# Performance work log

Hardware: AMD Instinct MI355X
Metric: run time of the kernel (lower is better)

Reference implementation:

```python
import jax, jax.numpy as jnp
import numpy as np

B, T, D, H = 64, 1024, 1, 256  # batch, seq_len, input_size(=output_size), hidden_size


def setup_inputs() -> dict:
    key = jax.random.key(0)
    ks = jax.random.split(key, 16)
    s = 1.0 / np.sqrt(H)  # torch LSTM/Linear default uniform init scale
    u = lambda k, shp: jax.random.uniform(k, shp, jnp.float32, -s, s)
    return {
        "x": jax.random.normal(ks[0], (B, T, D), jnp.float32),
        # encoder bidirectional 2-layer LSTM; leading dim 2 = (fwd, bwd); gate order i,f,g,o
        "enc_Wih_l0": u(ks[1], (2, 4 * H, D)),
        "enc_Whh_l0": u(ks[2], (2, 4 * H, H)),
        "enc_b_l0": u(ks[3], (2, 4 * H)),
        "enc_Wih_l1": u(ks[4], (2, 4 * H, 2 * H)),
        "enc_Whh_l1": u(ks[5], (2, 4 * H, H)),
        "enc_b_l1": u(ks[6], (2, 4 * H)),
        # decoder bidirectional 2-layer LSTM
        "dec_Wih_l0": u(ks[7], (2, 4 * H, D)),
        "dec_Whh_l0": u(ks[8], (2, 4 * H, H)),
        "dec_b_l0": u(ks[9], (2, 4 * H)),
        "dec_Wih_l1": u(ks[10], (2, 4 * H, 2 * H)),
        "dec_Whh_l1": u(ks[11], (2, 4 * H, H)),
        "dec_b_l1": u(ks[12], (2, 4 * H)),
        # output projection: Linear(2H -> 1)
        "fc_W": u(ks[13], (1, 2 * H)),
        "fc_b": u(ks[14], (1,)),
    }


def _cell(xt, h, c, Wih, Whh, b):
    # one LSTM cell step; xt: (B, Din), h/c: (B, H)
    gates = xt @ Wih.T + h @ Whh.T + b
    i, f, g, o = jnp.split(gates, 4, axis=-1)  # torch gate order i,f,g,o
    c = jax.nn.sigmoid(f) * c + jax.nn.sigmoid(i) * jnp.tanh(g)
    h = jax.nn.sigmoid(o) * jnp.tanh(c)
    return h, c


def _scan_dir(xs, Wih, Whh, b, reverse):
    # xs: (T, B, Din) time-major; returns (T,B,H) outputs aligned to input order + final (h,c)
    bsz = xs.shape[1]
    h0 = jnp.zeros((bsz, H), xs.dtype)
    def step(carry, xt):
        h, c = _cell(xt, carry[0], carry[1], Wih, Whh, b)
        return (h, c), h
    (hT, cT), ys = jax.lax.scan(step, (h0, h0), xs, reverse=reverse)
    return ys, hT, cT


def reference(x, enc_Wih_l0, enc_Whh_l0, enc_b_l0, enc_Wih_l1, enc_Whh_l1, enc_b_l1,
              dec_Wih_l0, dec_Whh_l0, dec_b_l0, dec_Wih_l1, dec_Whh_l1, dec_b_l1,
              fc_W, fc_b):
    xT = jnp.transpose(x, (1, 0, 2))  # (T, B, D)
    # ---- encoder: 2-layer bidirectional LSTM, zero initial state ----
    yf0, hf0, cf0 = _scan_dir(xT, enc_Wih_l0[0], enc_Whh_l0[0], enc_b_l0[0], False)
    yb0, hb0, cb0 = _scan_dir(xT, enc_Wih_l0[1], enc_Whh_l0[1], enc_b_l0[1], True)
    y0 = jnp.concatenate([yf0, yb0], axis=-1)  # (T, B, 2H)
    _, hf1, cf1 = _scan_dir(y0, enc_Wih_l1[0], enc_Whh_l1[0], enc_b_l1[0], False)
    _, hb1, cb1 = _scan_dir(y0, enc_Wih_l1[1], enc_Whh_l1[1], enc_b_l1[1], True)
    # torch state layout: [l0_fwd, l0_bwd, l1_fwd, l1_bwd]
    eh = (hf0, hb0, hf1, hb1)
    ec = (cf0, cb0, cf1, cb1)

    # ---- decoder: each step re-initializes LSTM state from ENCODER state (source bug,
    # reproduced faithfully); only the fc output feeds back as the next input ----
    def dec_step(x_in, _):
        hf, _c1 = _cell(x_in, eh[0], ec[0], dec_Wih_l0[0], dec_Whh_l0[0], dec_b_l0[0])
        hb, _c2 = _cell(x_in, eh[1], ec[1], dec_Wih_l0[1], dec_Whh_l0[1], dec_b_l0[1])
        z = jnp.concatenate([hf, hb], axis=-1)  # (B, 2H)
        hf1_, _c3 = _cell(z, eh[2], ec[2], dec_Wih_l1[0], dec_Whh_l1[0], dec_b_l1[0])
        hb1_, _c4 = _cell(z, eh[3], ec[3], dec_Wih_l1[1], dec_Whh_l1[1], dec_b_l1[1])
        y = jnp.concatenate([hf1_, hb1_], axis=-1) @ fc_W.T + fc_b  # (B, 1)
        return y, y

    x0 = jnp.zeros((x.shape[0], x.shape[2]), x.dtype)
    _, ys = jax.lax.scan(dec_step, x0, None, length=x.shape[1])  # (T, B, 1)
    return jnp.transpose(ys, (1, 0, 2))  # (B, T, 1)
```

## Files before the change

kernel.cpp:

```cpp
#include <hip/hip_runtime.h>
#include <hip/hip_bf16.h>
#include <hip/hip_fp16.h>
#include <math.h>


#define NWG 256
#define THR 512
#define U0S 132

#define ECL0   2048
#define EHL1   (ECL0 + 32768)
#define ECL1   (EHL1 + 16384)
#define ROF    (ECL1 + 32768)
#define WIH1T  (ROF + 262144)
#define GWR    (WIH1T + 524288)
#define PCF    (GWR + 1048576)
#define Y0OF   (PCF + 8192)
#define WS_REQ_BYTES ((size_t)(Y0OF + 16777216) * 4)

struct SeqParams {
  const void *x, *eWih0, *eWhh0, *eB0, *eWih1, *eWhh1, *eB1;
  const void *dWih0, *dWhh0, *dB0, *dWih1, *dWhh1, *dB1, *fcW, *fcb;
  void* out;
  float* ws;
  unsigned* ctrs;
};

typedef _Float16 hlf2 __attribute__((ext_vector_type(2)));

__device__ __forceinline__ float bf2f(unsigned short u) {
  return __uint_as_float(((unsigned)u) << 16);
}
__device__ __forceinline__ float hf2f(unsigned short u) {
  __half_raw r; r.x = u; return __half2float(__half(r));
}
__device__ __forceinline__ unsigned short f2h_u(float f) {
  __half h = __float2half(f);
  return *reinterpret_cast<unsigned short*>(&h);
}

__device__ __forceinline__ float fexp2(float x) {
#if __has_builtin(__builtin_amdgcn_exp2f)
  return __builtin_amdgcn_exp2f(x);
#else
  return exp2f(x);
#endif
}
__device__ __forceinline__ float frcp(float x) {
#if __has_builtin(__builtin_amdgcn_rcpf)
  return __builtin_amdgcn_rcpf(x);
#else
  return 1.0f / x;
#endif
}
__device__ __forceinline__ float sigm(float v) {
  return frcp(1.0f + fexp2(v * -1.44269504f));
}
__device__ __forceinline__ float ftanh(float v) {
  return fmaf(-2.0f, frcp(1.0f + fexp2(v * 2.88539008f)), 1.0f);
}

#if __has_builtin(__builtin_amdgcn_fdot2)
__device__ __forceinline__ float fdot2(hlf2 a, hlf2 b, float c) {
  return __builtin_amdgcn_fdot2(a, b, c, false);
}
#else
__device__ __forceinline__ float fdot2(hlf2 a, hlf2 b, float c) {
  return c + (float)a[0] * (float)b[0] + (float)a[1] * (float)b[1];
}
#endif

__device__ __forceinline__ float dot1(float a, const uint4& x, const uint4& y) {
  const hlf2* xp = reinterpret_cast<const hlf2*>(&x);
  const hlf2* yp = reinterpret_cast<const hlf2*>(&y);
  a = fdot2(xp[0], yp[0], a);
  a = fdot2(xp[1], yp[1], a);
  a = fdot2(xp[2], yp[2], a);
  a = fdot2(xp[3], yp[3], a);
  return a;
}
__device__ __forceinline__ void dot2acc(float4& a, const uint4& hv, const uint4& wv) {
  const hlf2* hp = reinterpret_cast<const hlf2*>(&hv);
  const hlf2* wp = reinterpret_cast<const hlf2*>(&wv);
  a.x = fdot2(hp[0], wp[0], a.x);
  a.y = fdot2(hp[1], wp[1], a.y);
  a.z = fdot2(hp[2], wp[2], a.z);
  a.w = fdot2(hp[3], wp[3], a.w);
}

__device__ __forceinline__ float ldin(const void* p_, size_t i, int bf) {
  return bf ? bf2f(((const unsigned short*)p_)[i]) : ((const float*)p_)[i];
}
__device__ __forceinline__ void stout(void* o, size_t i, float v, int bf) {
  if (bf) ((__hip_bfloat16*)o)[i] = __float2bfloat16(v);
  else    ((float*)o)[i] = v;
}

__device__ __forceinline__ int detect_bf16(const void* xp) {
  const unsigned* u = (const unsigned*)xp;
  int votes = 0;
#pragma unroll 8
  for (int i = 0; i < 64; ++i) {
    unsigned e = (u[i] >> 7) & 0xFF;
    votes += (e >= 108 && e <= 131) ? 1 : 0;
  }
  return votes >= 32;
}

__device__ __forceinline__ void gbar(unsigned* ctrs, unsigned gen) {
  __syncthreads();
  if (threadIdx.x == 0) {
    __hip_atomic_fetch_add(&ctrs[(blockIdx.x & 31) * 32], 1u,
                           __ATOMIC_RELEASE, __HIP_MEMORY_SCOPE_AGENT);
  }
  if (threadIdx.x < 32) {
    while (__hip_atomic_load(&ctrs[threadIdx.x * 32], __ATOMIC_RELAXED,
                             __HIP_MEMORY_SCOPE_AGENT) < gen * 8u) {
      __builtin_amdgcn_s_sleep(1);
    }
    (void)__hip_atomic_load(&ctrs[threadIdx.x * 32], __ATOMIC_ACQUIRE,
                            __HIP_MEMORY_SCOPE_AGENT);
  }
  __syncthreads();
}

__device__ __forceinline__ uint4 ldw8(const void* src, size_t off, int bf) {
  union { __half h[8]; uint4 u; } r;
  if (bf) {
    const unsigned short* s = (const unsigned short*)src + off;
    ushort4 a = *reinterpret_cast<const ushort4*>(s);
    ushort4 b = *reinterpret_cast<const ushort4*>(s + 4);
    r.h[0] = __float2half(bf2f(a.x)); r.h[1] = __float2half(bf2f(a.y));
    r.h[2] = __float2half(bf2f(a.z)); r.h[3] = __float2half(bf2f(a.w));
    r.h[4] = __float2half(bf2f(b.x)); r.h[5] = __float2half(bf2f(b.y));
    r.h[6] = __float2half(bf2f(b.z)); r.h[7] = __float2half(bf2f(b.w));
  } else {
    const float* s = (const float*)src + off;
    float4 a = *reinterpret_cast<const float4*>(s);
    float4 b = *reinterpret_cast<const float4*>(s + 4);
    r.h[0] = __float2half(a.x); r.h[1] = __float2half(a.y);
    r.h[2] = __float2half(a.z); r.h[3] = __float2half(a.w);
    r.h[4] = __float2half(b.x); r.h[5] = __float2half(b.y);
    r.h[6] = __float2half(b.z); r.h[7] = __float2half(b.w);
  }
  return r.u;
}

__device__ __forceinline__ void stage_u128(unsigned* AH, const unsigned* src,
                                           int ustr, int uoff) {
  const int t = threadIdx.x;
#pragma unroll
  for (int i = 0; i < 4; ++i) {
    int idx = t + i * THR;
    int r = idx >> 5, c4 = (idx & 31) << 2;
    uint4 v = *reinterpret_cast<const uint4*>(src + (size_t)r * ustr + uoff + c4);
    *reinterpret_cast<uint4*>(AH + r * U0S + c4) = v;
  }
}
__device__ __forceinline__ void load_w16_rows(uint4 (&wr)[2][4], const void* src,
                                              int rowbase, int bf) {
  const int t = threadIdx.x, kc = t >> 6, rt = t & 3;
#pragma unroll
  for (int j = 0; j < 2; ++j) {
    size_t rb = (size_t)(rowbase + rt * 2 + j) * 256 + kc * 32;
#pragma unroll
    for (int d = 0; d < 4; ++d) wr[j][d] = ldw8(src, rb + d * 8, bf);
  }
}
__device__ __forceinline__ void dot2_t4(float4* acc, const unsigned* A,
                                        const uint4 (&wr)[2][4]) {
  const int t = threadIdx.x;
  const int kc = t >> 6, bt = (t & 63) >> 2;
#pragma unroll
  for (int d = 0; d < 4; ++d) {
    const int k = kc * 16 + d * 4;
    uint4 h0 = *reinterpret_cast<const uint4*>(A + (bt +  0) * U0S + k);
    uint4 h1 = *reinterpret_cast<const uint4*>(A + (bt + 16) * U0S + k);
    uint4 h2 = *reinterpret_cast<const uint4*>(A + (bt + 32) * U0S + k);
    uint4 h3 = *reinterpret_cast<const uint4*>(A + (bt + 48) * U0S + k);
    dot2acc(acc[0], h0, wr[0][d]); dot2acc(acc[1], h0, wr[1][d]);
    dot2acc(acc[2], h1, wr[0][d]); dot2acc(acc[3], h1, wr[1][d]);
    dot2acc(acc[4], h2, wr[0][d]); dot2acc(acc[5], h2, wr[1][d]);
    dot2acc(acc[6], h3, wr[0][d]); dot2acc(acc[7], h3, wr[1][d]);
  }
}
__device__ __forceinline__ void reduce_R(const float4* acc, float* part, float* dst,
                                         const void* bsrc, int rowbase, int bf) {
  const int t = threadIdx.x;
  const int kc = t >> 6, tile = t & 63;
#pragma unroll
  for (int e = 0; e < 8; ++e) {
    const float4 a = acc[e];
    part[e * 512 + kc * 64 + tile] = (a.x + a.y) + (a.z + a.w);
  }
  __syncthreads();
  {
    const int r = t >> 6, b = t & 63;
    const int tl = (b & 15) * 4 + (r >> 1);
    const float* pp = part + ((b >> 4) * 2 + (r & 1)) * 512 + tl;
    float v = ((pp[0] + pp[64]) + (pp[128] + pp[192])) +
              ((pp[256] + pp[320]) + (pp[384] + pp[448]));
    dst[(size_t)b * 1024 + rowbase + r] = v + ldin(bsrc, rowbase + r, bf);
  }
  __syncthreads();
}

__global__ void __launch_bounds__(THR, 2)
__attribute__((amdgpu_waves_per_eu(2, 2)))
seq2seq_kernel(SeqParams p) {
  __shared__ __align__(16) char smem[148736];
  uint4* WLDSu4 = (uint4*)smem;
  float* GF     = (float*)(smem + 131072);
  float* PREB   = (float*)(smem + 135168);
  float* PREWf  = (float*)(smem + 139264);
  float* XROW   = (float*)(smem + 143360);
  unsigned* H16 = (unsigned*)(smem + 147456);
  float* YL     = (float*)(smem + 148480);

  const int w = blockIdx.x;
  const int t = threadIdx.x;
  float* ws = p.ws;
  unsigned* ctrs = p.ctrs;
  unsigned* y0w   = (unsigned*)(ws + Y0OF);
  unsigned* EHL1u = (unsigned*)(ws + EHL1);
  uint4* WIH1Tu4  = (uint4*)(ws + WIH1T);
  unsigned* GWu   = (unsigned*)(ws + GWR);
  unsigned* flg   = (unsigned*)(ws + PCF);
  uint4* DWu4     = (uint4*)(ws + Y0OF);
  unsigned genF = 0;
  const int bfm = detect_bf16(p.x);
  const int enc_act = (w < 128);
  const int d = (w >> 6) & 1, b = w & 63;
  const int R0 = t >> 1, hs = t & 1, swz = R0 & 7;

  uint4 wreg3[3][16];

  {
    if (w == 0) {
      for (int i = t; i < 8192; i += THR) flg[i] = 0u;
    }
    if (enc_act) {
      const void* whh0 = bfm ? (const void*)((const unsigned short*)p.eWhh0 + (size_t)d * 262144)
                             : (const void*)((const float*)p.eWhh0 + (size_t)d * 262144);
#pragma unroll
      for (int kk = 0; kk < 16; ++kk) {
        wreg3[0][kk] = ldw8(whh0, (size_t)R0 * 256 + (size_t)hs * 128 + kk * 8, bfm);
        wreg3[1][kk] = ldw8(whh0, (size_t)(256 + R0) * 256 + (size_t)hs * 128 + kk * 8, bfm);
        wreg3[2][kk] = ldw8(whh0, (size_t)(512 + R0) * 256 + (size_t)hs * 128 + kk * 8, bfm);
      }
#pragma unroll
      for (int i = 0; i < 16; ++i) {
        int idx = t + i * 512;
        int row = idx >> 5, j = idx & 31;
        WLDSu4[row * 32 + (j ^ (row & 7))] =
            ldw8(whh0, (size_t)(768 + row) * 256 + j * 8, bfm);
      }
#pragma unroll
      for (int q = 0; q < 2; ++q) {
        PREB[t + q * 512]  = ldin(p.eB0,   d * 1024 + t + q * 512, bfm);
        PREWf[t + q * 512] = ldin(p.eWih0, d * 1024 + t + q * 512, bfm);
        XROW[t + q * 512]  = ldin(p.x, (size_t)b * 1024 + t + q * 512, bfm);
      }
      if (t < 256) H16[t] = 0u;
    }
  }
  gbar(ctrs, ++genF);

  if (enc_act) {
    float cc = 0.f;
    const uint4* wl = WLDSu4 + R0 * 32;
    int pp = 0;
    for (int st = 0; st < 1024; ++st) {
      const int tt = d ? (1023 - st) : st;
      float s0 = 0.f, s1 = 0.f, s2 = 0.f, s3 = 0.f;
      const unsigned* hb = H16 + pp * 128 + hs * 64;
#pragma unroll
      for (int i = 0; i < 16; ++i) {
        uint4 hv = *(const uint4*)(hb + i * 4);
        s0 = dot1(s0, hv, wreg3[0][i]);
        s1 = dot1(s1, hv, wreg3[1][i]);
        s2 = dot1(s2, hv, wreg3[2][i]);
        s3 = dot1(s3, hv, wl[(hs * 16 + i) ^ swz]);
      }
      s0 += __shfl_xor(s0, 1, 64);
      s1 += __shfl_xor(s1, 1, 64);
      s2 += __shfl_xor(s2, 1, 64);
      s3 += __shfl_xor(s3, 1, 64);
      float xv = XROW[tt];
      float gi = s0 + PREB[R0]       + xv * PREWf[R0];
      float gf = s1 + PREB[256 + R0] + xv * PREWf[256 + R0];
      float gg = s2 + PREB[512 + R0] + xv * PREWf[512 + R0];
      float go = s3 + PREB[768 + R0] + xv * PREWf[768 + R0];
      float cn = sigm(gf) * cc + sigm(gi) * ftanh(gg);
      float hn = sigm(go) * ftanh(cn);
      cc = cn;
      unsigned hu = (unsigned)f2h_u(hn);
      unsigned hnn = __shfl_down(hu, 2, 64);
      if ((t & 3) == 0)
        y0w[(size_t)tt * 16384 + (size_t)b * 256 + d * 128 + (t >> 2)] =
            hu | (hnn << 16);
      if (hs == 0) ((unsigned short*)(H16 + (pp ^ 1) * 128))[R0] = (unsigned short)hu;
      if (st == 1023 && hs == 0) ws[ECL0 + d * 16384 + b * 256 + R0] = cn;
      __syncthreads();
      pp ^= 1;
    }
  }
  gbar(ctrs, ++genF);

  {
    {
      int idx = w * 512 + t;
      int dd = idx >> 16, rem = idx & 65535;
      int kc = rem >> 10, row = rem & 1023;
      WIH1Tu4[idx] = ldw8(p.eWih1, (size_t)dd * 524288 + (size_t)row * 512 + kc * 8, bfm);
    }
    if (enc_act) {
      const void* whh1 = bfm ? (const void*)((const unsigned short*)p.eWhh1 + (size_t)d * 262144)
                             : (const void*)((const float*)p.eWhh1 + (size_t)d * 262144);
#pragma unroll
      for (int kk = 0; kk < 16; ++kk) {
        wreg3[0][kk] = ldw8(whh1, (size_t)R0 * 256 + (size_t)hs * 128 + kk * 8, bfm);
        wreg3[1][kk] = ldw8(whh1, (size_t)(256 + R0) * 256 + (size_t)hs * 128 + kk * 8, bfm);
        wreg3[2][kk] = ldw8(whh1, (size_t)(512 + R0) * 256 + (size_t)hs * 128 + kk * 8, bfm);
      }
#pragma unroll
      for (int i = 0; i < 16; ++i) {
        int idx = t + i * 512;
        int row = idx >> 5, j = idx & 31;
        WLDSu4[row * 32 + (j ^ (row & 7))] =
            ldw8(whh1, (size_t)(768 + row) * 256 + j * 8, bfm);
      }
#pragma unroll
      for (int q = 0; q < 2; ++q)
        PREB[t + q * 512] = ldin(p.eB1, d * 1024 + t + q * 512, bfm);
      if (t < 256) H16[t] = 0u;
    }
  }
  gbar(ctrs, ++genF);

  if (enc_act) {
    float cc = 0.f;
    const uint4* wl = WLDSu4 + R0 * 32;
    int pp = 0;
    for (int st = 0; st < 1024; ++st) {
      const int win = st >> 3, sl = st & 7;
      if (sl == 0) {
        if (t == 0) {
          while (__hip_atomic_load(&flg[w * 64], __ATOMIC_RELAXED,
                                   __HIP_MEMORY_SCOPE_AGENT) < (unsigned)(win + 1)) {
            __builtin_amdgcn_s_sleep(1);
          }
        }
        __atomic_signal_fence(__ATOMIC_ACQUIRE);
        __syncthreads();
      }
      const unsigned gb = (unsigned)w * 8192 + (unsigned)(win & 1) * 4096 + (unsigned)sl * 512;
      unsigned gw0 = __hip_atomic_load(&GWu[gb + R0],       __ATOMIC_RELAXED, __HIP_MEMORY_SCOPE_AGENT);
      unsigned gw1 = __hip_atomic_load(&GWu[gb + 256 + R0], __ATOMIC_RELAXED, __HIP_MEMORY_SCOPE_AGENT);
      float s0 = 0.f, s1 = 0.f, s2 = 0.f, s3 = 0.f;
      const unsigned* hb = H16 + pp * 128 + hs * 64;
#pragma unroll
      for (int i = 0; i < 16; ++i) {
        uint4 hv = *(const uint4*)(hb + i * 4);
        s0 = dot1(s0, hv, wreg3[0][i]);
        s1 = dot1(s1, hv, wreg3[1][i]);
        s2 = dot1(s2, hv, wreg3[2][i]);
        s3 = dot1(s3, hv, wl[(hs * 16 + i) ^ swz]);
      }
      s0 += __shfl_xor(s0, 1, 64);
      s1 += __shfl_xor(s1, 1, 64);
      s2 += __shfl_xor(s2, 1, 64);
      s3 += __shfl_xor(s3, 1, 64);
      float gi = s0 + PREB[R0]       + hf2f((unsigned short)(gw0 & 0xffffu));
      float gf = s1 + PREB[256 + R0] + hf2f((unsigned short)(gw1 & 0xffffu));
      float gg = s2 + PREB[512 + R0] + hf2f((unsigned short)(gw0 >> 16));
      float go = s3 + PREB[768 + R0] + hf2f((unsigned short)(gw1 >> 16));
      float cn = sigm(gf) * cc + sigm(gi) * ftanh(gg);
      float hn = sigm(go) * ftanh(cn);
      cc = cn;
      unsigned hu = (unsigned)f2h_u(hn);
      unsigned hnn = __shfl_down(hu, 2, 64);
      if (st == 1023) {
        if ((t & 3) == 0)
          EHL1u[d * 8192 + b * 128 + (t >> 2)] = hu | (hnn << 16);
        if (hs == 0) ws[ECL1 + d * 16384 + b * 256 + R0] = cn;
      }
      if (hs == 0) ((unsigned short*)(H16 + (pp ^ 1) * 128))[R0] = (unsigned short)hu;
      __syncthreads();
      if (sl == 7 && t == 0)
        __hip_atomic_store(&flg[w * 64 + 32], (unsigned)(win + 1),
                           __ATOMIC_RELAXED, __HIP_MEMORY_SCOPE_AGENT);
      pp ^= 1;
    }
  } else {
    const int chain = w - 128, dp = chain >> 6, bp = chain & 63;
    const uint4* Wt = WIH1Tu4 + (size_t)dp * 65536;
    uint4* YWu4 = (uint4*)smem;
    for (int win = 0; win < 128; ++win) {
      if (win >= 2) {
        if (t == 0) {
          while (__hip_atomic_load(&flg[chain * 64 + 32], __ATOMIC_RELAXED,
                                   __HIP_MEMORY_SCOPE_AGENT) < (unsigned)(win - 1)) {
            __builtin_amdgcn_s_sleep(1);
          }
        }
        __syncthreads();
      }
      {
        int s = t >> 6, kcc = t & 63;
        int tw = dp ? (1023 - (win * 8 + s)) : (win * 8 + s);
        YWu4[s * 64 + kcc] =
            *(const uint4*)(y0w + (size_t)tw * 16384 + (size_t)bp * 256 + kcc * 4);
      }
      __syncthreads();
      float a0[8], a1[8];
#pragma unroll
      for (int s = 0; s < 8; ++s) { a0[s] = 0.f; a1[s] = 0.f; }
      for (int kc = 0; kc < 64; ++kc) {
        uint4 w0 = Wt[kc * 1024 + t];
        uint4 w1 = Wt[kc * 1024 + 512 + t];
#pragma unroll
        for (int s = 0; s < 8; ++s) {
          uint4 yv = YWu4[s * 64 + kc];
          a0[s] = dot1(a0[s], yv, w0);
          a1[s] = dot1(a1[s], yv, w1);
        }
      }
      const unsigned gb = (unsigned)chain * 8192 + (unsigned)(win & 1) * 4096;
#pragma unroll
      for (int s = 0; s < 8; ++s) {
        unsigned pw = (unsigned)f2h_u(a0[s]) | ((unsigned)f2h_u(a1[s]) << 16);
        __hip_atomic_store(&GWu[gb + s * 512 + t], pw,
                           __ATOMIC_RELAXED, __HIP_MEMORY_SCOPE_AGENT);
      }
      __syncthreads();
      if (t == 0)
        __hip_atomic_store(&flg[chain * 64], (unsigned)(win + 1),
                           __ATOMIC_RELAXED, __HIP_MEMORY_SCOPE_AGENT);
    }
  }
  gbar(ctrs, ++genF);

  {
    unsigned* AH0 = (unsigned*)smem;
    float* part = (float*)(smem + 33792);
    const int m = w >> 6, wl6 = w & 63;
    const void* whh;
    if (bfm) whh = (m < 2) ? (const void*)((const unsigned short*)p.dWhh0 + (size_t)m * 262144)
                           : (const void*)((const unsigned short*)p.dWhh1 + (size_t)(m - 2) * 262144);
    else     whh = (m < 2) ? (const void*)((const float*)p.dWhh0 + (size_t)m * 262144)
                           : (const void*)((const float*)p.dWhh1 + (size_t)(m - 2) * 262144);
    const void* bb;
    if (bfm) bb = (m < 2) ? (const void*)((const unsigned short*)p.dB0 + m * 1024)
                          : (const void*)((const unsigned short*)p.dB1 + (m - 2) * 1024);
    else     bb = (m < 2) ? (const void*)((const float*)p.dB0 + m * 1024)
                          : (const void*)((const float*)p.dB1 + (m - 2) * 1024);
    if (m == 0)      stage_u128(AH0, y0w + (size_t)1023 * 16384, 256, 0);
    else if (m == 1) stage_u128(AH0, y0w, 256, 128);
    else             stage_u128(AH0, EHL1u + (m - 2) * 8192, 128, 0);
    __syncthreads();
    float* dst = ws + ROF + m * 65536;
    for (int pass = 0; pass < 2; ++pass) {
      const int rowbase = wl6 * 16 + pass * 8;
      uint4 wrA[2][4];
      load_w16_rows(wrA, whh, rowbase, bfm);
      float4 acc[8];
#pragma unroll
      for (int e = 0; e < 8; ++e) acc[e] = make_float4(0.f, 0.f, 0.f, 0.f);
      dot2_t4(acc, AH0, wrA);
      reduce_R(acc, part, dst, bb, rowbase, bfm);
    }
  }
  gbar(ctrs, ++genF);

  {
    int idx = w * 512 + t;
    int dd = idx >> 16, rem = idx & 65535;
    int kc = rem >> 10, row = rem & 1023;
    DWu4[idx] = ldw8(p.dWih1, (size_t)dd * 524288 + (size_t)row * 512 + kc * 8, bfm);
  }
  float r1i = 0.f, r1f = 0.f, r1g = 0.f, r1o = 0.f, coldc = 0.f, fwc = 0.f, fcb = 0.f;
  {
    float* R0L  = (float*)smem;
    float* WI0L = (float*)(smem + 8192);
    float* C0L  = (float*)(smem + 16384);
    if (w < 64) {
      const int bq = w;
#pragma unroll
      for (int i = 0; i < 4; ++i) {
        int r = t + i * THR;
        int dz = r >> 10, rr = r & 1023;
        R0L[r]  = ws[ROF + dz * 65536 + (size_t)bq * 1024 + rr];
        WI0L[r] = ldin(p.dWih0, dz * 1024 + rr, bfm);
      }
      C0L[t >= 512 ? 0 : t] = ws[ECL0 + (t >> 8) * 16384 + (size_t)bq * 256 + (t & 255)];
      const int dd2 = t >> 8, col = t & 255;
      r1i = ws[ROF + (2 + dd2) * 65536 + (size_t)bq * 1024 +       col];
      r1f = ws[ROF + (2 + dd2) * 65536 + (size_t)bq * 1024 + 256 + col];
      r1g = ws[ROF + (2 + dd2) * 65536 + (size_t)bq * 1024 + 512 + col];
      r1o = ws[ROF + (2 + dd2) * 65536 + (size_t)bq * 1024 + 768 + col];
      coldc = ws[ECL1 + dd2 * 16384 + (size_t)bq * 256 + col];
      fwc = ldin(p.fcW, dd2 * 256 + col, bfm);
      fcb = ldin(p.fcb, 0, bfm);
    }
  }
  gbar(ctrs, ++genF);

  if (w < 64) {
    const int bq = w;
    float* R0L  = (float*)smem;
    float* WI0L = (float*)(smem + 8192);
    float* C0L  = (float*)(smem + 16384);
    unsigned* ZV = (unsigned*)(smem + 18432);
    const int dd2 = t >> 8, col = t & 255;
    const uint4* DWt = DWu4 + (size_t)dd2 * 65536;

    {
      float gi = R0L[dd2 * 1024 +       col];
      float gf = R0L[dd2 * 1024 + 256 + col];
      float gg = R0L[dd2 * 1024 + 512 + col];
      float go = R0L[dd2 * 1024 + 768 + col];
      float cold = C0L[dd2 * 256 + col];
      float cn = sigm(gf) * cold + sigm(gi) * ftanh(gg);
      float hz = sigm(go) * ftanh(cn);
      ((unsigned short*)ZV)[t] = f2h_u(hz);
    }
    __syncthreads();

    float yp1 = 3.0e38f, yp2 = -3.0e38f;
    for (int st = 0; st < 1024; ++st) {
      float ai = 0.f, af = 0.f, ag = 0.f, ao = 0.f;
      for (int kc = 0; kc < 64; ++kc) {
        uint4 zv = *(const uint4*)(ZV + kc * 4);
        uint4 w0 = DWt[kc * 1024 +       col];
        uint4 w1 = DWt[kc * 1024 + 256 + col];
        uint4 w2 = DWt[kc * 1024 + 512 + col];
        uint4 w3 = DWt[kc * 1024 + 768 + col];
        ai = dot1(ai, zv, w0);
        af = dot1(af, zv, w1);
        ag = dot1(ag, zv, w2);
        ao = dot1(ao, zv, w3);
      }
      float gi = ai + r1i, gf = af + r1f, gg = ag + r1g, go = ao + r1o;
      float cn = sigm(gf) * coldc + sigm(gi) * ftanh(gg);
      float h1 = sigm(go) * ftanh(cn);
      GF[t] = h1 * fwc;
      __syncthreads();
      if (t < 64) {
        const float* q = GF + t;
        GF[t] = ((q[0] + q[64]) + (q[128] + q[192])) +
                ((q[256] + q[320]) + (q[384] + q[448]));
      }
      __syncthreads();
      if (t == 0) {
        float yy = fcb;
        for (int i = 0; i < 64; ++i) yy += GF[i];
        YL[0] = yy;
      }
      __syncthreads();
      float ynew = YL[0];
      if (t == 0) stout(p.out, (size_t)bq * 1024 + st, ynew, bfm);
      if (ynew == yp1) {
        for (int t2 = st + 1 + t; t2 < 1024; t2 += THR)
          stout(p.out, (size_t)bq * 1024 + t2, ynew, bfm);
        break;
      }
      if (ynew == yp2) {
        for (int t2 = st + 1 + t; t2 < 1024; t2 += THR)
          stout(p.out, (size_t)bq * 1024 + t2, ((t2 - st) & 1) ? yp1 : ynew, bfm);
        break;
      }
      yp2 = yp1; yp1 = ynew;
      if (st < 1023) {
        __syncthreads();
        float gi2 = ynew * WI0L[dd2 * 1024 +       col] + R0L[dd2 * 1024 +       col];
        float gf2 = ynew * WI0L[dd2 * 1024 + 256 + col] + R0L[dd2 * 1024 + 256 + col];
        float gg2 = ynew * WI0L[dd2 * 1024 + 512 + col] + R0L[dd2 * 1024 + 512 + col];
        float go2 = ynew * WI0L[dd2 * 1024 + 768 + col] + R0L[dd2 * 1024 + 768 + col];
        float cold = C0L[dd2 * 256 + col];
        float cn2 = sigm(gf2) * cold + sigm(gi2) * ftanh(gg2);
        float hz = sigm(go2) * ftanh(cn2);
        ((unsigned short*)ZV)[t] = f2h_u(hz);
        __syncthreads();
      }
    }
  }
}

__global__ void fill_sig(unsigned short* out, int n, float val) {
  int i = blockIdx.x * 256 + threadIdx.x;
  __hip_bfloat16 b = __float2bfloat16(val);
  if (i < n) out[i] = *reinterpret_cast<unsigned short*>(&b);
}

extern "C" void kernel_launch(void* const* d_in, const int* in_sizes, int n_in,
                              void* d_out, int out_size, void* d_ws, size_t ws_size,
                              hipStream_t stream) {
  (void)in_sizes; (void)n_in;
  if (ws_size < WS_REQ_BYTES) {
    float sig = 2048.0f + (float)(ws_size >> 20);
    fill_sig<<<(out_size + 255) / 256, 256, 0, stream>>>(
        (unsigned short*)d_out, out_size, sig);
    return;
  }
  hipMemsetAsync(d_ws, 0, 8192, stream);

  SeqParams p;
  p.x     = d_in[0];
  p.eWih0 = d_in[1];
  p.eWhh0 = d_in[2];
  p.eB0   = d_in[3];
  p.eWih1 = d_in[4];
  p.eWhh1 = d_in[5];
  p.eB1   = d_in[6];
  p.dWih0 = d_in[7];
  p.dWhh0 = d_in[8];
  p.dB0   = d_in[9];
  p.dWih1 = d_in[10];
  p.dWhh1 = d_in[11];
  p.dB1   = d_in[12];
  p.fcW   = d_in[13];
  p.fcb   = d_in[14];
  p.out   = d_out;
  p.ws    = (float*)d_ws;
  p.ctrs  = (unsigned*)d_ws;

  seq2seq_kernel<<<dim3(NWG), dim3(THR), 0, stream>>>(p);
}
```

Before: 5.955 ms.

## Use MFMA for encoder recurrent matvec and prefetch Wih1 during layer-0

Replaces the per-thread fdot2 recurrent h·Whh dot products in both encoder layers with 16x16x32 f16 MFMA instructions. Weight fragments are held in registers (6 tiles) and LDS (2 tiles), and the gate pre-activations are staged through LDS so 256 threads run the cell update. Layer-0 y0 stores are deferred one step so they overlap the next step's compute. The idle decoder-side blocks now transpose Wih1 before layer 0 instead of between layers, taking that work off the critical path. In exchange, each step gains an extra LDS round trip and barrier, and the MFMA computes mostly-wasted columns because the batch dimension per block is 1.

```diff
diff --git a/kernel.cpp b/kernel.cpp
--- a/kernel.cpp
+++ b/kernel.cpp
@@ -27,6 +27,8 @@
 };
 
 typedef _Float16 hlf2 __attribute__((ext_vector_type(2)));
+typedef _Float16 half8 __attribute__((ext_vector_type(8)));
+typedef float floatx4 __attribute__((ext_vector_type(4)));
 
 __device__ __forceinline__ float bf2f(unsigned short u) {
   return __uint_as_float(((unsigned)u) << 16);
@@ -86,6 +88,12 @@
   a.y = fdot2(hp[1], wp[1], a.y);
   a.z = fdot2(hp[2], wp[2], a.z);
   a.w = fdot2(hp[3], wp[3], a.w);
+}
+
+__device__ __forceinline__ floatx4 mfma16(uint4 a, uint4 b, floatx4 c) {
+  union { uint4 u; half8 h; } ua, ub;
+  ua.u = a; ub.u = b;
+  return __builtin_amdgcn_mfma_f32_16x16x32_f16(ua.h, ub.h, c, 0, 0, 0);
 }
 
 __device__ __forceinline__ float ldin(const void* p_, size_t i, int bf) {
@@ -209,7 +217,7 @@
 __attribute__((amdgpu_waves_per_eu(2, 2)))
 seq2seq_kernel(SeqParams p) {
   __shared__ __align__(16) char smem[148736];
-  uint4* WLDSu4 = (uint4*)smem;
+  uint4* FRAGu4 = (uint4*)smem;
   float* GF     = (float*)(smem + 131072);
   float* PREB   = (float*)(smem + 135168);
   float* PREWf  = (float*)(smem + 139264);
@@ -231,9 +239,10 @@
   const int bfm = detect_bf16(p.x);
   const int enc_act = (w < 128);
   const int d = (w >> 6) & 1, b = w & 63;
-  const int R0 = t >> 1, hs = t & 1, swz = R0 & 7;
-
-  uint4 wreg3[3][16];
+  const int wv = t >> 6, l = t & 63;
+  const int lg = l >> 4, lr = l & 15;
+
+  uint4 awr[6][8];
 
   {
     if (w == 0) {
@@ -243,18 +252,17 @@
       const void* whh0 = bfm ? (const void*)((const unsigned short*)p.eWhh0 + (size_t)d * 262144)
                              : (const void*)((const float*)p.eWhh0 + (size_t)d * 262144);
 #pragma unroll
-      for (int kk = 0; kk < 16; ++kk) {
-        wreg3[0][kk] = ldw8(whh0, (size_t)R0 * 256 + (size_t)hs * 128 + kk * 8, bfm);
-        wreg3[1][kk] = ldw8(whh0, (size_t)(256 + R0) * 256 + (size_t)hs * 128 + kk * 8, bfm);
-        wreg3[2][kk] = ldw8(whh0, (size_t)(512 + R0) * 256 + (size_t)hs * 128 + kk * 8, bfm);
-      }
-#pragma unroll
-      for (int i = 0; i < 16; ++i) {
-        int idx = t + i * 512;
-        int row = idx >> 5, j = idx & 31;
-        WLDSu4[row * 32 + (j ^ (row & 7))] =
-            ldw8(whh0, (size_t)(768 + row) * 256 + j * 8, bfm);
-      }
+      for (int mt = 0; mt < 6; ++mt)
+#pragma unroll
+        for (int kc = 0; kc < 8; ++kc)
+          awr[mt][kc] = ldw8(whh0,
+              (size_t)(wv * 128 + mt * 16 + lr) * 256 + kc * 32 + lg * 8, bfm);
+#pragma unroll
+      for (int mt2 = 0; mt2 < 2; ++mt2)
+#pragma unroll
+        for (int kc = 0; kc < 8; ++kc)
+          FRAGu4[(wv * 16 + mt2 * 8 + kc) * 64 + l] = ldw8(whh0,
+              (size_t)(wv * 128 + (6 + mt2) * 16 + lr) * 256 + kc * 32 + lg * 8, bfm);
 #pragma unroll
       for (int q = 0; q < 2; ++q) {
         PREB[t + q * 512]  = ldin(p.eB0,   d * 1024 + t + q * 512, bfm);
@@ -262,74 +270,91 @@
         XROW[t + q * 512]  = ldin(p.x, (size_t)b * 1024 + t + q * 512, bfm);
       }
       if (t < 256) H16[t] = 0u;
+    } else {
+#pragma unroll
+      for (int q = 0; q < 2; ++q) {
+        int idx = (w - 128) * 1024 + q * 512 + t;
+        int dd = idx >> 16, rem = idx & 65535;
+        int kc = rem >> 10, row = rem & 1023;
+        WIH1Tu4[idx] = ldw8(p.eWih1, (size_t)dd * 524288 + (size_t)row * 512 + kc * 8, bfm);
+      }
     }
   }
   gbar(ctrs, ++genF);
 
   if (enc_act) {
     float cc = 0.f;
-    const uint4* wl = WLDSu4 + R0 * 32;
     int pp = 0;
+    unsigned ppw = 0;
+    int ptt = -1;
     for (int st = 0; st < 1024; ++st) {
       const int tt = d ? (1023 - st) : st;
-      float s0 = 0.f, s1 = 0.f, s2 = 0.f, s3 = 0.f;
-      const unsigned* hb = H16 + pp * 128 + hs * 64;
-#pragma unroll
-      for (int i = 0; i < 16; ++i) {
-        uint4 hv = *(const uint4*)(hb + i * 4);
-        s0 = dot1(s0, hv, wreg3[0][i]);
-        s1 = dot1(s1, hv, wreg3[1][i]);
-        s2 = dot1(s2, hv, wreg3[2][i]);
-        s3 = dot1(s3, hv, wl[(hs * 16 + i) ^ swz]);
-      }
-      s0 += __shfl_xor(s0, 1, 64);
-      s1 += __shfl_xor(s1, 1, 64);
-      s2 += __shfl_xor(s2, 1, 64);
-      s3 += __shfl_xor(s3, 1, 64);
-      float xv = XROW[tt];
-      float gi = s0 + PREB[R0]       + xv * PREWf[R0];
-      float gf = s1 + PREB[256 + R0] + xv * PREWf[256 + R0];
-      float gg = s2 + PREB[512 + R0] + xv * PREWf[512 + R0];
-      float go = s3 + PREB[768 + R0] + xv * PREWf[768 + R0];
-      float cn = sigm(gf) * cc + sigm(gi) * ftanh(gg);
-      float hn = sigm(go) * ftanh(cn);
-      cc = cn;
-      unsigned hu = (unsigned)f2h_u(hn);
-      unsigned hnn = __shfl_down(hu, 2, 64);
-      if ((t & 3) == 0)
-        y0w[(size_t)tt * 16384 + (size_t)b * 256 + d * 128 + (t >> 2)] =
-            hu | (hnn << 16);
-      if (hs == 0) ((unsigned short*)(H16 + (pp ^ 1) * 128))[R0] = (unsigned short)hu;
-      if (st == 1023 && hs == 0) ws[ECL0 + d * 16384 + b * 256 + R0] = cn;
+      if (ptt >= 0 && t < 256 && !(t & 1))
+        y0w[(size_t)ptt * 16384 + (size_t)b * 256 + d * 128 + (t >> 1)] = ppw;
+      float xv = (t < 256) ? XROW[tt] : 0.f;
+      floatx4 acc[8];
+#pragma unroll
+      for (int m = 0; m < 8; ++m) acc[m] = (floatx4){0.f, 0.f, 0.f, 0.f};
+      const uint4* hb4 = (const uint4*)(H16 + pp * 128);
+#pragma unroll
+      for (int kc = 0; kc < 8; ++kc) {
+        uint4 bu = hb4[kc * 4 + lg];
+        uint4 a6 = FRAGu4[(wv * 16 + kc) * 64 + l];
+        uint4 a7 = FRAGu4[(wv * 16 + 8 + kc) * 64 + l];
+        acc[0] = mfma16(awr[0][kc], bu, acc[0]);
+        acc[1] = mfma16(awr[1][kc], bu, acc[1]);
+        acc[2] = mfma16(awr[2][kc], bu, acc[2]);
+        acc[3] = mfma16(awr[3][kc], bu, acc[3]);
+        acc[4] = mfma16(awr[4][kc], bu, acc[4]);
+        acc[5] = mfma16(awr[5][kc], bu, acc[5]);
+        acc[6] = mfma16(a6, bu, acc[6]);
+        acc[7] = mfma16(a7, bu, acc[7]);
+      }
+      if (lr == 0) {
+#pragma unroll
+        for (int m = 0; m < 8; ++m)
+          *reinterpret_cast<floatx4*>(GF + wv * 128 + m * 16 + lg * 4) = acc[m];
+      }
+      __syncthreads();
+      if (t < 256) {
+        float gi = GF[t]       + PREB[t]       + xv * PREWf[t];
+        float gf = GF[256 + t] + PREB[256 + t] + xv * PREWf[256 + t];
+        float gg = GF[512 + t] + PREB[512 + t] + xv * PREWf[512 + t];
+        float go = GF[768 + t] + PREB[768 + t] + xv * PREWf[768 + t];
+        float cn = sigm(gf) * cc + sigm(gi) * ftanh(gg);
+        float hn = sigm(go) * ftanh(cn);
+        cc = cn;
+        unsigned hu = (unsigned)f2h_u(hn);
+        ((unsigned short*)(H16 + (pp ^ 1) * 128))[t] = (unsigned short)hu;
+        unsigned nn = __shfl_down(hu, 1, 64);
+        if (!(t & 1)) ppw = hu | (nn << 16);
+        ptt = tt;
+        if (st == 1023) ws[ECL0 + d * 16384 + b * 256 + t] = cn;
+      }
       __syncthreads();
       pp ^= 1;
     }
+    if (ptt >= 0 && t < 256 && !(t & 1))
+      y0w[(size_t)ptt * 16384 + (size_t)b * 256 + d * 128 + (t >> 1)] = ppw;
   }
   gbar(ctrs, ++genF);
 
   {
-    {
-      int idx = w * 512 + t;
-      int dd = idx >> 16, rem = idx & 65535;
-      int kc = rem >> 10, row = rem & 1023;
-      WIH1Tu4[idx] = ldw8(p.eWih1, (size_t)dd * 524288 + (size_t)row * 512 + kc * 8, bfm);
-    }
     if (enc_act) {
       const void* whh1 = bfm ? (const void*)((const unsigned short*)p.eWhh1 + (size_t)d * 262144)
                              : (const void*)((const float*)p.eWhh1 + (size_t)d * 262144);
 #pragma unroll
-      for (int kk = 0; kk < 16; ++kk) {
-        wreg3[0][kk] = ldw8(whh1, (size_t)R0 * 256 + (size_t)hs * 128 + kk * 8, bfm);
-        wreg3[1][kk] = ldw8(whh1, (size_t)(256 + R0) * 256 + (size_t)hs * 128 + kk * 8, bfm);
-        wreg3[2][kk] = ldw8(whh1, (size_t)(512 + R0) * 256 + (size_t)hs * 128 + kk * 8, bfm);
-      }
-#pragma unroll
-      for (int i = 0; i < 16; ++i) {
-        int idx = t + i * 512;
-        int row = idx >> 5, j = idx & 31;
-        WLDSu4[row * 32 + (j ^ (row & 7))] =
-            ldw8(whh1, (size_t)(768 + row) * 256 + j * 8, bfm);
-      }
+      for (int mt = 0; mt < 6; ++mt)
+#pragma unroll
+        for (int kc = 0; kc < 8; ++kc)
+          awr[mt][kc] = ldw8(whh1,
+              (size_t)(wv * 128 + mt * 16 + lr) * 256 + kc * 32 + lg * 8, bfm);
+#pragma unroll
+      for (int mt2 = 0; mt2 < 2; ++mt2)
+#pragma unroll
+        for (int kc = 0; kc < 8; ++kc)
+          FRAGu4[(wv * 16 + mt2 * 8 + kc) * 64 + l] = ldw8(whh1,
+              (size_t)(wv * 128 + (6 + mt2) * 16 + lr) * 256 + kc * 32 + lg * 8, bfm);
 #pragma unroll
       for (int q = 0; q < 2; ++q)
         PREB[t + q * 512] = ldin(p.eB1, d * 1024 + t + q * 512, bfm);
@@ -340,7 +365,6 @@
 
   if (enc_act) {
     float cc = 0.f;
-    const uint4* wl = WLDSu4 + R0 * 32;
     int pp = 0;
     for (int st = 0; st < 1024; ++st) {
       const int win = st >> 3, sl = st & 7;
@@ -354,38 +378,53 @@
         __atomic_signal_fence(__ATOMIC_ACQUIRE);
         __syncthreads();
       }
-      const unsigned gb = (unsigned)w * 8192 + (unsigned)(win & 1) * 4096 + (unsigned)sl * 512;
-      unsigned gw0 = __hip_atomic_load(&GWu[gb + R0],       __ATOMIC_RELAXED, __HIP_MEMORY_SCOPE_AGENT);
-      unsigned gw1 = __hip_atomic_load(&GWu[gb + 256 + R0], __ATOMIC_RELAXED, __HIP_MEMORY_SCOPE_AGENT);
-      float s0 = 0.f, s1 = 0.f, s2 = 0.f, s3 = 0.f;
-      const unsigned* hb = H16 + pp * 128 + hs * 64;
-#pragma unroll
-      for (int i = 0; i < 16; ++i) {
-        uint4 hv = *(const uint4*)(hb + i * 4);
-        s0 = dot1(s0, hv, wreg3[0][i]);
-        s1 = dot1(s1, hv, wreg3[1][i]);
-        s2 = dot1(s2, hv, wreg3[2][i]);
-        s3 = dot1(s3, hv, wl[(hs * 16 + i) ^ swz]);
-      }
-      s0 += __shfl_xor(s0, 1, 64);
-      s1 += __shfl_xor(s1, 1, 64);
-      s2 += __shfl_xor(s2, 1, 64);
-      s3 += __shfl_xor(s3, 1, 64);
-      float gi = s0 + PREB[R0]       + hf2f((unsigned short)(gw0 & 0xffffu));
-      float gf = s1 + PREB[256 + R0] + hf2f((unsigned short)(gw1 & 0xffffu));
-      float gg = s2 + PREB[512 + R0] + hf2f((unsigned short)(gw0 >> 16));
-      float go = s3 + PREB[768 + R0] + hf2f((unsigned short)(gw1 >> 16));
-      float cn = sigm(gf) * cc + sigm(gi) * ftanh(gg);
-      float hn = sigm(go) * ftanh(cn);
-      cc = cn;
-      unsigned hu = (unsigned)f2h_u(hn);
-      unsigned hnn = __shfl_down(hu, 2, 64);
-      if (st == 1023) {
-        if ((t & 3) == 0)
-          EHL1u[d * 8192 + b * 128 + (t >> 2)] = hu | (hnn << 16);
-        if (hs == 0) ws[ECL1 + d * 16384 + b * 256 + R0] = cn;
-      }
-      if (hs == 0) ((unsigned short*)(H16 + (pp ^ 1) * 128))[R0] = (unsigned short)hu;
+      unsigned gw0 = 0, gw1 = 0;
+      if (t < 256) {
+        const unsigned gb = (unsigned)w * 8192 + (unsigned)(win & 1) * 4096 + (unsigned)sl * 512;
+        gw0 = __hip_atomic_load(&GWu[gb + t],       __ATOMIC_RELAXED, __HIP_MEMORY_SCOPE_AGENT);
+        gw1 = __hip_atomic_load(&GWu[gb + 256 + t], __ATOMIC_RELAXED, __HIP_MEMORY_SCOPE_AGENT);
+      }
+      floatx4 acc[8];
+#pragma unroll
+      for (int m = 0; m < 8; ++m) acc[m] = (floatx4){0.f, 0.f, 0.f, 0.f};
+      const uint4* hb4 = (const uint4*)(H16 + pp * 128);
+#pragma unroll
+      for (int kc = 0; kc < 8; ++kc) {
+        uint4 bu = hb4[kc * 4 + lg];
+        uint4 a6 = FRAGu4[(wv * 16 + kc) * 64 + l];
+        uint4 a7 = FRAGu4[(wv * 16 + 8 + kc) * 64 + l];
+        acc[0] = mfma16(awr[0][kc], bu, acc[0]);
+        acc[1] = mfma16(awr[1][kc], bu, acc[1]);
+        acc[2] = mfma16(awr[2][kc], bu, acc[2]);
+        acc[3] = mfma16(awr[3][kc], bu, acc[3]);
+        acc[4] = mfma16(awr[4][kc], bu, acc[4]);
+        acc[5] = mfma16(awr[5][kc], bu, acc[5]);
+        acc[6] = mfma16(a6, bu, acc[6]);
+        acc[7] = mfma16(a7, bu, acc[7]);
+      }
+      if (lr == 0) {
+#pragma unroll
+        for (int m = 0; m < 8; ++m)
+          *reinterpret_cast<floatx4*>(GF + wv * 128 + m * 16 + lg * 4) = acc[m];
+      }
+      __syncthreads();
+      if (t < 256) {
+        float gi = GF[t]       + PREB[t]       + hf2f((unsigned short)(gw0 & 0xffffu));
+        float gf = GF[256 + t] + PREB[256 + t] + hf2f((unsigned short)(gw1 & 0xffffu));
+        float gg = GF[512 + t] + PREB[512 + t] + hf2f((unsigned short)(gw0 >> 16));
+        float go = GF[768 + t] + PREB[768 + t] + hf2f((unsigned short)(gw1 >> 16));
+        float cn = sigm(gf) * cc + sigm(gi) * ftanh(gg);
+        float hn = sigm(go) * ftanh(cn);
+        cc = cn;
+        unsigned hu = (unsigned)f2h_u(hn);
+        ((unsigned short*)(H16 + (pp ^ 1) * 128))[t] = (unsigned short)hu;
+        if (st == 1023) {
+          unsigned nn = __shfl_down(hu, 1, 64);
+          if (!(t & 1))
+            EHL1u[d * 8192 + b * 128 + (t >> 1)] = hu | (nn << 16);
+          ws[ECL1 + d * 16384 + b * 256 + t] = cn;
+        }
+      }
       __syncthreads();
       if (sl == 7 && t == 0)
         __hip_atomic_store(&flg[w * 64 + 32], (unsigned)(win + 1),
```

Result: slower. 6.131 ms (+2.9%).
